# Optimization experiments

Hardware: AMD Instinct MI355X
Metric: run time of the kernel (lower is better)

The kernel has to match this reference:

```python
import jax, jax.numpy as jnp
import numpy as np

B, T, C = 2, 2048, 4096
NH, NKV, HD = 32, 8, 128
GROUPS = NH // NKV
THETA = 10000.0


def _rope_tables(seq_len, dim, theta, dtype):
    inv_freq = 1.0 / (theta ** (jnp.arange(0, dim, 2, dtype=jnp.float32) / dim))
    t = jnp.arange(seq_len, dtype=jnp.float32)
    freqs = jnp.outer(t, inv_freq)            # [T, dim/2]
    emb = jnp.concatenate([freqs, freqs], -1)  # [T, dim]
    return jnp.cos(emb).astype(dtype), jnp.sin(emb).astype(dtype)


def _rotate_half(x):
    h = x.shape[-1] // 2
    return jnp.concatenate([-x[..., h:], x[..., :h]], axis=-1)


def setup_inputs() -> dict:
    key = jax.random.key(0)
    ks = jax.random.split(key, 5)
    s = 1.0 / np.sqrt(C)
    return {
        "x": jax.random.normal(ks[0], (B, T, C), jnp.float32),
        "wq": jax.random.normal(ks[1], (C, NH * HD), jnp.float32) * s,
        "wk": jax.random.normal(ks[2], (C, NKV * HD), jnp.float32) * s,
        "wv": jax.random.normal(ks[3], (C, NKV * HD), jnp.float32) * s,
        "wo": jax.random.normal(ks[4], (NH * HD, C), jnp.float32) * s,
    }


def reference(x, wq, wk, wv, wo):
    b, t, c = x.shape
    q = (x @ wq).reshape(b, t, NH, HD).transpose(0, 2, 1, 3)    # [B,NH,T,HD]
    k = (x @ wk).reshape(b, t, NKV, HD).transpose(0, 2, 1, 3)   # [B,NKV,T,HD]
    v = (x @ wv).reshape(b, t, NKV, HD).transpose(0, 2, 1, 3)
    cos, sin = _rope_tables(t, HD, THETA, x.dtype)              # [T,HD]
    cos = cos[None, None]
    sin = sin[None, None]
    q = q * cos + _rotate_half(q) * sin
    k = k * cos + _rotate_half(k) * sin
    # GQA: broadcast KV heads over groups via einsum instead of materializing repeat
    qg = q.reshape(b, NKV, GROUPS, t, HD)
    scores = jnp.einsum('bkgqd,bkld->bkgql', qg, k) * (HD ** -0.5)  # [B,NKV,G,T,T]
    causal = jnp.triu(jnp.full((t, t), -jnp.inf, dtype=x.dtype), k=1)
    scores = scores + causal
    attn = jax.nn.softmax(scores, axis=-1)
    out = jnp.einsum('bkgql,bkld->bkgqd', attn, v)              # [B,NKV,G,T,HD]
    out = out.reshape(b, NH, t, HD).transpose(0, 2, 1, 3).reshape(b, t, NH * HD)
    return out @ wo
```

## Files before the change

kernel.cpp:

```cpp
#include <hip/hip_runtime.h>
#include <hip/hip_bf16.h>
#include <math.h>

#define B_ 2
#define T_ 2048
#define C_ 4096
#define NH_ 32
#define NKV_ 8
#define HD_ 128
#define M_ (B_*T_)
#define QKVN_ (NH_*HD_ + 2*NKV_*HD_)

using bf16 = __hip_bfloat16;
typedef __bf16 bf16x8 __attribute__((ext_vector_type(8)));
typedef float f32x4 __attribute__((ext_vector_type(4)));

__device__ inline f32x4 mfma16(bf16x8 a, bf16x8 b, f32x4 c) {
    return __builtin_amdgcn_mfma_f32_16x16x32_bf16(a, b, c, 0, 0, 0);
}

__global__ __launch_bounds__(256) void cast_f32_bf16(const float* __restrict__ in,
                                                     bf16* __restrict__ out, int n4) {
    int i = blockIdx.x * 256 + threadIdx.x;
    if (i >= n4) return;
    float4 v = reinterpret_cast<const float4*>(in)[i];
    union { bf16 h[4]; uint2 u; } o;
    o.h[0] = __float2bfloat16(v.x);
    o.h[1] = __float2bfloat16(v.y);
    o.h[2] = __float2bfloat16(v.z);
    o.h[3] = __float2bfloat16(v.w);
    reinterpret_cast<uint2*>(out)[i] = o.u;
}

__global__ __launch_bounds__(256) void transpose_cast(const float* __restrict__ in,
                                                      bf16* __restrict__ out, int K, int N) {
    __shared__ float tile[32][33];
    int tx = threadIdx.x & 31, ty = threadIdx.x >> 5;
    int n0 = blockIdx.x << 5, k0 = blockIdx.y << 5;
#pragma unroll
    for (int p = 0; p < 4; ++p)
        tile[p*8 + ty][tx] = in[(size_t)(k0 + p*8 + ty) * N + n0 + tx];
    __syncthreads();
#pragma unroll
    for (int p = 0; p < 4; ++p)
        out[(size_t)(n0 + p*8 + ty) * K + k0 + tx] = __float2bfloat16(tile[tx][p*8 + ty]);
}

__device__ inline void store_out(float* p, float v) { *p = v; }
__device__ inline void store_out(bf16*  p, float v) { *p = __float2bfloat16(v); }

template <typename OutT>
__global__ __launch_bounds__(512, 2) void gemm256(const bf16* __restrict__ A,
                                                  const bf16* __restrict__ Bt,
                                                  OutT* __restrict__ C,
                                                  int M, int N, int K) {
    __shared__ __align__(16) char lds[131072];
    const int tid = threadIdx.x;
    const int wid = tid >> 6, lane = tid & 63;
    const int lq = lane & 15, lg = lane >> 4;
    const int wrow = wid >> 2, wcol = wid & 3;

    const int nwg = gridDim.x;
    const int q8 = nwg >> 3;
    const int wg = (blockIdx.x & 7) * q8 + (blockIdx.x >> 3);
    const int nby = M >> 8;
    const int by = wg % nby, bx = wg / nby;
    const int brow = by << 8, bcol = bx << 8;

    const bf16* Ag = A + (size_t)brow * K;
    const bf16* Bg = Bt + (size_t)bcol * K;
    const int nt = K >> 6;

    const int srow = (wid << 3) + (lane >> 3);
    const int schunk = (lane & 7) ^ ((lane >> 3) & 7);

#define STAGE_HALF(gbase, ldsoff, t2, cbuf, hf)                                         \
    {                                                                                   \
        _Pragma("unroll")                                                               \
        for (int l = 0; l < 2; ++l) {                                                   \
            const int r0 = (hf) * 128 + l * 64;                                         \
            const char* src = (const char*)(gbase) +                                    \
                ((size_t)(r0 + srow) * K + (size_t)(t2) * 64) * 2 + schunk * 16;        \
            char* dst = &lds[(ldsoff) + (cbuf) * 32768 + (r0 + (wid << 3)) * 128];      \
            __builtin_amdgcn_global_load_lds(                                           \
                (const __attribute__((address_space(1))) void*)src,                     \
                (__attribute__((address_space(3))) void*)dst, 16, 0, 0);                \
        }                                                                               \
    }

#define LDA(cbuf, mh, mf, ks) \
    (*(const bf16x8*)&lds[(cbuf)*32768 + (wrow*128 + (mh)*64 + (mf)*16 + lq)*128 + ((((ks)*4 + lg)) ^ (lq & 7))*16])
#define LDB(cbuf, nh, nf, ks) \
    (*(const bf16x8*)&lds[65536 + (cbuf)*32768 + (wcol*64 + (nh)*32 + (nf)*16 + lq)*128 + ((((ks)*4 + lg)) ^ (lq & 7))*16])

#define READ_A(cbuf, mh) \
    { _Pragma("unroll") for (int mf = 0; mf < 4; ++mf) { a[mf][0] = LDA(cbuf, mh, mf, 0); a[mf][1] = LDA(cbuf, mh, mf, 1); } }
#define READ_B(cbuf, nh, breg) \
    { _Pragma("unroll") for (int nf = 0; nf < 2; ++nf) { breg[nf][0] = LDB(cbuf, nh, nf, 0); breg[nf][1] = LDB(cbuf, nh, nf, 1); } }
#define MFMA_Q(am, an, breg)                                                     \
    { __builtin_amdgcn_s_setprio(1);                                             \
      _Pragma("unroll") for (int mf = 0; mf < 4; ++mf)                           \
          _Pragma("unroll") for (int nf = 0; nf < 2; ++nf)                       \
              _Pragma("unroll") for (int ks = 0; ks < 2; ++ks)                   \
                  acc[(am) + mf][(an) + nf] = mfma16(a[mf][ks], breg[nf][ks],    \
                                                     acc[(am) + mf][(an) + nf]); \
      __builtin_amdgcn_s_setprio(0); }
#define BAR() __builtin_amdgcn_s_barrier()

    f32x4 acc[8][4] = {};
    bf16x8 a[4][2], b0[2][2], b1[2][2];

    STAGE_HALF(Ag, 0,     0, 0, 0); STAGE_HALF(Ag, 0,     0, 0, 1);
    STAGE_HALF(Bg, 65536, 0, 0, 0); STAGE_HALF(Bg, 65536, 0, 0, 1);
    STAGE_HALF(Bg, 65536, 1, 1, 0); STAGE_HALF(Bg, 65536, 1, 1, 1);
    asm volatile("s_waitcnt vmcnt(4)" ::: "memory");
    BAR();

    for (int i = 0; i < (nt >> 1); ++i) {
        const int u = 2 * i;
        const bool s_u2 = (u + 2) < nt;
        const bool s_v2 = (u + 3) < nt;

        READ_A(0, 0); READ_B(0, 0, b0);
        STAGE_HALF(Ag, 0, u + 1, 1, 0);
        MFMA_Q(0, 0, b0);
        BAR();
        READ_B(0, 1, b1);
        STAGE_HALF(Ag, 0, u + 1, 1, 1);
        MFMA_Q(0, 2, b1);
        BAR();
        READ_A(0, 1);
        if (s_u2) STAGE_HALF(Bg, 65536, u + 2, 0, 0);
        MFMA_Q(4, 2, b1);
        BAR();
        if (s_u2) STAGE_HALF(Bg, 65536, u + 2, 0, 1);
        MFMA_Q(4, 0, b0);
        if (s_u2) asm volatile("s_waitcnt vmcnt(4)" ::: "memory");
        else      asm volatile("s_waitcnt vmcnt(0)" ::: "memory");
        BAR();
        READ_A(1, 0); READ_B(1, 0, b0);
        if (s_u2) STAGE_HALF(Ag, 0, u + 2, 0, 0);
        MFMA_Q(0, 0, b0);
        BAR();
        READ_B(1, 1, b1);
        if (s_u2) STAGE_HALF(Ag, 0, u + 2, 0, 1);
        MFMA_Q(0, 2, b1);
        BAR();
        READ_A(1, 1);
        if (s_v2) STAGE_HALF(Bg, 65536, u + 3, 1, 0);
        MFMA_Q(4, 2, b1);
        BAR();
        if (s_v2) STAGE_HALF(Bg, 65536, u + 3, 1, 1);
        MFMA_Q(4, 0, b0);
        if (s_v2) asm volatile("s_waitcnt vmcnt(4)" ::: "memory");
        else      asm volatile("s_waitcnt vmcnt(0)" ::: "memory");
        BAR();
    }
#undef STAGE_HALF
#undef LDA
#undef LDB
#undef READ_A
#undef READ_B
#undef MFMA_Q
#undef BAR

#pragma unroll
    for (int mf = 0; mf < 8; ++mf)
#pragma unroll
        for (int nf = 0; nf < 4; ++nf)
#pragma unroll
            for (int r = 0; r < 4; ++r) {
                int row = brow + wrow * 128 + mf * 16 + lg * 4 + r;
                int col = bcol + wcol * 64 + nf * 16 + lq;
                store_out(&C[(size_t)row * N + col], acc[mf][nf][r]);
            }
}

__global__ __launch_bounds__(256) void rope_qk(const bf16* __restrict__ qkv,
                                               bf16* __restrict__ outp,
                                               int nheads, int col_off, float qscale) {
    size_t idx = (size_t)blockIdx.x * 256 + threadIdx.x;
    int i = (int)(idx & 63);
    size_t rest = idx >> 6;
    int t = (int)(rest % T_);
    rest /= T_;
    int hh = (int)(rest % nheads);
    int b = (int)(rest / nheads);

    const bf16* src = qkv + (size_t)(b * T_ + t) * QKVN_ + col_off + hh * HD_;
    float x0 = __bfloat162float(src[i]);
    float x1 = __bfloat162float(src[i + 64]);
    float inv = exp2f((float)i * -0.20762050593045952f);
    float th = (float)t * inv;
    float s = sinf(th), c = cosf(th);
    bf16* dst = outp + ((size_t)(b * nheads + hh) * T_ + t) * HD_;
    dst[i]      = __float2bfloat16((x0 * c - x1 * s) * qscale);
    dst[i + 64] = __float2bfloat16((x1 * c + x0 * s) * qscale);
}

__global__ __launch_bounds__(256) void vtrans(const bf16* __restrict__ qkv,
                                              bf16* __restrict__ vt) {
    __shared__ bf16 tile[32][33];
    int gx = blockIdx.x;
    int dt = gx & 3;
    int tt = (gx >> 2) & 63;
    int kv = (gx >> 8) & 7;
    int b  = gx >> 11;
    int d0 = dt * 32, t0 = tt * 32;
    int tx = threadIdx.x & 31, ty = threadIdx.x >> 5;

    const bf16* src = qkv + (size_t)(b * T_ + t0) * QKVN_ + (NH_*HD_ + NKV_*HD_) + kv * HD_ + d0;
#pragma unroll
    for (int p = 0; p < 4; ++p)
        tile[p*8 + ty][tx] = src[(size_t)(p*8 + ty) * QKVN_ + tx];
    __syncthreads();
    bf16* dst = vt + ((size_t)((b * NKV_ + kv) * HD_ + d0)) * T_ + t0;
#pragma unroll
    for (int p = 0; p < 4; ++p)
        dst[(size_t)(p*8 + ty) * T_ + tx] = tile[tx][p*8 + ty];
}

__global__ __launch_bounds__(1024) void fattn(const bf16* __restrict__ Q,
                                              const bf16* __restrict__ Kt,
                                              const bf16* __restrict__ VT,
                                              bf16* __restrict__ O) {
    const int lin = blockIdx.x;
    const int kv = lin & 7;
    const int b  = (lin >> 3) & 1;
    const int idx = lin >> 4;
    const int h  = kv * 4 + (idx & 3);
    const int jp = idx >> 2;

    const int tid = threadIdx.x, wid = tid >> 6, lane = tid & 63;
    const int lq = lane & 15, lg = lane >> 4;

    const bf16* Kp = Kt + (size_t)(b * NKV_ + kv) * T_ * HD_;
    const bf16* Vp = VT + (size_t)(b * NKV_ + kv) * HD_ * T_;

    __shared__ __align__(16) bf16 Ks[2][64][128];
    __shared__ __align__(16) bf16 Vs[2][128][64];
    __shared__ __align__(16) bf16 p_lds[16][16][72];

    const float THR_L2 = 11.5416f;

#define STAGE_KV(cbuf, tt)                                                           \
    { {                                                                              \
        int krow = wid * 4 + (lane >> 4);                                            \
        int kch  = (lane & 15) ^ (krow & 15);                                        \
        const bf16* ksrc = Kp + (size_t)((tt) * 64 + krow) * HD_ + kch * 8;          \
        __builtin_amdgcn_global_load_lds(                                            \
            (const __attribute__((address_space(1))) void*)ksrc,                     \
            (__attribute__((address_space(3))) void*)&Ks[cbuf][wid*4][0],            \
            16, 0, 0);                                                               \
      }                                                                              \
      {                                                                              \
        int vrow = wid * 8 + (lane >> 3);                                            \
        int vch  = (lane & 7) ^ (vrow & 7);                                          \
        const bf16* vsrc = Vp + (size_t)vrow * T_ + (tt) * 64 + vch * 8;             \
        __builtin_amdgcn_global_load_lds(                                            \
            (const __attribute__((address_space(1))) void*)vsrc,                     \
            (__attribute__((address_space(3))) void*)&Vs[cbuf][wid*8][0],            \
            16, 0, 0);                                                               \
      } }

    for (int half = 0; half < 2; ++half) {
        const int qt = half ? (7 - jp) : jp;
        const int q0 = qt * 256 + wid * 16;
        const int kv_end = q0 + 16;
        const int NT = qt * 4 + 4;

        const bf16* Qp = Q + ((size_t)(b * NH_ + h) * T_ + q0) * HD_;
        bf16x8 qf[4];
#pragma unroll
        for (int c = 0; c < 4; ++c)
            qf[c] = *(const bf16x8*)&Qp[(size_t)lq * HD_ + c * 32 + lg * 8];

        f32x4 oacc[8] = {};
        float m_r = -INFINITY;
        float l_r = 0.f;

        STAGE_KV(0, 0);
        STAGE_KV(1, 1);
        asm volatile("s_waitcnt vmcnt(2)" ::: "memory");
        __builtin_amdgcn_s_barrier();

        for (int t = 0; t < NT; ++t) {
            const int cb = t & 1;
            const int t0 = t * 64;

            if (t0 < kv_end) {
                f32x4 st[4] = {};
#pragma unroll
                for (int n = 0; n < 4; ++n) {
                    bf16x8 kf[4];
#pragma unroll
                    for (int c = 0; c < 4; ++c)
                        kf[c] = *(const bf16x8*)((const char*)&Ks[cb][n*16 + lq][0]
                                                  + (((c*4 + lg) ^ lq) << 4));
                    __builtin_amdgcn_s_setprio(1);
#pragma unroll
                    for (int c = 0; c < 4; ++c)
                        st[n] = mfma16(kf[c], qf[c], st[n]);
                    __builtin_amdgcn_s_setprio(0);
                }

                const int qq = q0 + lq;
#pragma unroll
                for (int n = 0; n < 4; ++n)
#pragma unroll
                    for (int r = 0; r < 4; ++r) {
                        int kk = t0 + n*16 + lg*4 + r;
                        if (kk > qq) st[n][r] = -INFINITY;
                    }

                float rmax = st[0][0];
#pragma unroll
                for (int n = 0; n < 4; ++n)
#pragma unroll
                    for (int r = 0; r < 4; ++r) rmax = fmaxf(rmax, st[n][r]);
                rmax = fmaxf(rmax, __shfl_xor(rmax, 16));
                rmax = fmaxf(rmax, __shfl_xor(rmax, 32));

                if (__any(rmax - m_r > THR_L2)) {
                    float mnew = fmaxf(m_r, rmax);
                    float alpha = exp2f(m_r - mnew);
                    m_r = mnew;
                    l_r *= alpha;
#pragma unroll
                    for (int r = 0; r < 4; ++r) {
                        float a_pv = __shfl(alpha, lg*4 + r);
#pragma unroll
                        for (int f = 0; f < 8; ++f) oacc[f][r] *= a_pv;
                    }
                }

                float rsum = 0.f;
#pragma unroll
                for (int n = 0; n < 4; ++n)
#pragma unroll
                    for (int r = 0; r < 4; ++r) {
                        float p = exp2f(st[n][r] - m_r);
                        st[n][r] = p;
                        rsum += p;
                    }
                rsum += __shfl_xor(rsum, 16);
                rsum += __shfl_xor(rsum, 32);
                l_r += rsum;

#pragma unroll
                for (int n = 0; n < 4; ++n) {
                    union { bf16 hh[4]; uint2 u; } pk;
#pragma unroll
                    for (int r = 0; r < 4; ++r) pk.hh[r] = __float2bfloat16(st[n][r]);
                    *(uint2*)&p_lds[wid][lq][n*16 + lg*4] = pk.u;
                }

#pragma unroll
                for (int ks = 0; ks < 2; ++ks) {
                    bf16x8 pa = *(const bf16x8*)&p_lds[wid][lq][ks*32 + lg*8];
                    bf16x8 vf[8];
#pragma unroll
                    for (int f = 0; f < 8; ++f)
                        vf[f] = *(const bf16x8*)((const char*)&Vs[cb][f*16 + lq][0]
                                                  + (((ks*4 + lg) ^ (lq & 7)) << 4));
                    __builtin_amdgcn_s_setprio(1);
#pragma unroll
                    for (int f = 0; f < 8; ++f)
                        oacc[f] = mfma16(pa, vf[f], oacc[f]);
                    __builtin_amdgcn_s_setprio(0);
                }
            }

            __builtin_amdgcn_s_barrier();
            if (t + 2 < NT) {
                STAGE_KV(cb, t + 2);
                asm volatile("s_waitcnt vmcnt(2)" ::: "memory");
            } else {
                asm volatile("s_waitcnt vmcnt(0)" ::: "memory");
            }
            __builtin_amdgcn_s_barrier();
        }

        {
            float rinv = __builtin_amdgcn_rcpf(l_r);
#pragma unroll
            for (int r = 0; r < 4; ++r) {
                float rl = __shfl(rinv, lg*4 + r);
                int row = q0 + lg*4 + r;
#pragma unroll
                for (int f = 0; f < 8; ++f) {
                    int d = f*16 + lq;
                    O[((size_t)(b * T_ + row) * NH_ + h) * HD_ + d] =
                        __float2bfloat16(oacc[f][r] * rl);
                }
            }
        }
    }
#undef STAGE_KV
}

extern "C" void kernel_launch(void* const* d_in, const int* in_sizes, int n_in,
                              void* d_out, int out_size, void* d_ws, size_t ws_size,
                              hipStream_t stream) {
    const float* x  = (const float*)d_in[0];
    const float* wq = (const float*)d_in[1];
    const float* wk = (const float*)d_in[2];
    const float* wv = (const float*)d_in[3];
    const float* wo = (const float*)d_in[4];
    float* out = (float*)d_out;

    bf16* ws    = (bf16*)d_ws;
    bf16* xb    = ws;
    bf16* wqkvT = xb + (size_t)M_ * C_;
    bf16* woT   = wqkvT + (size_t)QKVN_ * C_;
    bf16* qkv   = woT + (size_t)C_ * C_;

    bf16* attn = xb;
    bf16* q_r  = wqkvT;
    bf16* k_r  = q_r + (size_t)B_ * NH_ * T_ * HD_;
    bf16* vt   = k_r + (size_t)B_ * NKV_ * T_ * HD_;

    cast_f32_bf16<<<(M_ * C_ / 4 + 255) / 256, 256, 0, stream>>>(x, xb, M_ * C_ / 4);
    transpose_cast<<<dim3(128, 128), 256, 0, stream>>>(wq, wqkvT, C_, NH_ * HD_);
    transpose_cast<<<dim3(32, 128), 256, 0, stream>>>(wk, wqkvT + (size_t)(NH_ * HD_) * C_, C_, NKV_ * HD_);
    transpose_cast<<<dim3(32, 128), 256, 0, stream>>>(wv, wqkvT + (size_t)(NH_ * HD_ + NKV_ * HD_) * C_, C_, NKV_ * HD_);
    transpose_cast<<<dim3(128, 128), 256, 0, stream>>>(wo, woT, NH_ * HD_, C_);

    gemm256<bf16><<<dim3((QKVN_ / 256) * (M_ / 256)), 512, 0, stream>>>(xb, wqkvT, qkv, M_, QKVN_, C_);

    rope_qk<<<(B_ * NH_ * T_ * 64) / 256, 256, 0, stream>>>(qkv, q_r, NH_, 0, 0.12751741230963214f);
    rope_qk<<<(B_ * NKV_ * T_ * 64) / 256, 256, 0, stream>>>(qkv, k_r, NKV_, NH_ * HD_, 1.0f);
    vtrans<<<B_ * NKV_ * (T_ / 32) * (HD_ / 32), 256, 0, stream>>>(qkv, vt);

    fattn<<<dim3(256), 1024, 0, stream>>>(q_r, k_r, vt, attn);

    gemm256<float><<<dim3((C_ / 256) * (M_ / 256)), 512, 0, stream>>>(attn, woT, out, M_, C_, C_);
}
```

Baseline: 521.7 us.

## Fuse RoPE into QKV GEMM epilogue and deepen GEMM prefetch waits

Adds a gemm_qkv kernel that remaps the B-tile columns so each wave holds both halves of a rotary pair. RoPE and the query scale are applied in the epilogue, which writes Q and K straight to head-major layout, and V goes to a compact buffer. This removes the separate rope_qk passes and the full bf16 QKV round trip, and a small precomputed cos/sin table replaces per-element trig. The shared GEMM loop now waits on vmcnt(8) instead of vmcnt(4), allowing more loads in flight. The wo transpose moves after attention so its buffer can be reused for Q, and the scattered epilogue stores may be less coalesced.

After: 502.0 us. 3.8% less time.

```diff
diff --git a/kernel.cpp b/kernel.cpp
--- a/kernel.cpp
+++ b/kernel.cpp
@@ -46,32 +46,79 @@
         out[(size_t)(n0 + p*8 + ty) * K + k0 + tx] = __float2bfloat16(tile[tx][p*8 + ty]);
 }
 
-__device__ inline void store_out(float* p, float v) { *p = v; }
-__device__ inline void store_out(bf16*  p, float v) { *p = __float2bfloat16(v); }
-
-template <typename OutT>
-__global__ __launch_bounds__(512, 2) void gemm256(const bf16* __restrict__ A,
-                                                  const bf16* __restrict__ Bt,
-                                                  OutT* __restrict__ C,
-                                                  int M, int N, int K) {
-    __shared__ __align__(16) char lds[131072];
-    const int tid = threadIdx.x;
-    const int wid = tid >> 6, lane = tid & 63;
-    const int lq = lane & 15, lg = lane >> 4;
-    const int wrow = wid >> 2, wcol = wid & 3;
-
-    const int nwg = gridDim.x;
-    const int q8 = nwg >> 3;
-    const int wg = (blockIdx.x & 7) * q8 + (blockIdx.x >> 3);
-    const int nby = M >> 8;
-    const int by = wg % nby, bx = wg / nby;
-    const int brow = by << 8, bcol = bx << 8;
-
-    const bf16* Ag = A + (size_t)brow * K;
-    const bf16* Bg = Bt + (size_t)bcol * K;
-    const int nt = K >> 6;
-
-    const int srow = (wid << 3) + (lane >> 3);
+__global__ __launch_bounds__(256) void rope_tab(float2* __restrict__ tab) {
+    int idx = blockIdx.x * 256 + threadIdx.x;
+    int i = idx & 63, t = idx >> 6;
+    float inv = exp2f((float)i * -0.20762050593045952f);
+    float th = (float)t * inv;
+    tab[idx] = make_float2(cosf(th), sinf(th));
+}
+
+#define GEMM_PROLOG_AND_LOOP(LDB_ROW_EXPR)                                              \
+    f32x4 acc[8][4] = {};                                                               \
+    bf16x8 a[4][2], b0[2][2], b1[2][2];                                                 \
+    STAGE_HALF(Ag, 0,     0, 0, 0); STAGE_HALF(Ag, 0,     0, 0, 1);                     \
+    STAGE_HALF(Bg, 65536, 0, 0, 0); STAGE_HALF(Bg, 65536, 0, 0, 1);                     \
+    STAGE_HALF(Bg, 65536, 1, 1, 0); STAGE_HALF(Bg, 65536, 1, 1, 1);                     \
+    asm volatile("s_waitcnt vmcnt(4)" ::: "memory");                                    \
+    BAR();                                                                              \
+    for (int it = 0; it < (nt >> 1); ++it) {                                            \
+        const int u = 2 * it;                                                           \
+        const bool more = (u + 2) < nt;                                                 \
+        READ_A(0, 0); READ_B(0, 0, b0);                                                 \
+        STAGE_HALF(Ag, 0, u + 1, 1, 0);                                                 \
+        MFMA_Q(0, 0, b0);                                                               \
+        BAR();                                                                          \
+        READ_B(0, 1, b1);                                                               \
+        STAGE_HALF(Ag, 0, u + 1, 1, 1);                                                 \
+        MFMA_Q(0, 2, b1);                                                               \
+        BAR();                                                                          \
+        READ_A(0, 1);                                                                   \
+        if (more) STAGE_HALF(Bg, 65536, u + 2, 0, 0);                                   \
+        MFMA_Q(4, 2, b1);                                                               \
+        BAR();                                                                          \
+        if (more) STAGE_HALF(Bg, 65536, u + 2, 0, 1);                                   \
+        MFMA_Q(4, 0, b0);                                                               \
+        if (more) asm volatile("s_waitcnt vmcnt(8)" ::: "memory");                      \
+        else      asm volatile("s_waitcnt vmcnt(4)" ::: "memory");                      \
+        BAR();                                                                          \
+        READ_A(1, 0); READ_B(1, 0, b0);                                                 \
+        if (more) STAGE_HALF(Ag, 0, u + 2, 0, 0);                                       \
+        MFMA_Q(0, 0, b0);                                                               \
+        BAR();                                                                          \
+        READ_B(1, 1, b1);                                                               \
+        if (more) STAGE_HALF(Ag, 0, u + 2, 0, 1);                                       \
+        MFMA_Q(0, 2, b1);                                                               \
+        if (more) asm volatile("s_waitcnt vmcnt(8)" ::: "memory");                      \
+        else      asm volatile("s_waitcnt vmcnt(0)" ::: "memory");                      \
+        BAR();                                                                          \
+        READ_A(1, 1);                                                                   \
+        if (more) STAGE_HALF(Bg, 65536, u + 3, 1, 0);                                   \
+        MFMA_Q(4, 2, b1);                                                               \
+        BAR();                                                                          \
+        if (more) STAGE_HALF(Bg, 65536, u + 3, 1, 1);                                   \
+        MFMA_Q(4, 0, b0);                                                               \
+        if (more) asm volatile("s_waitcnt vmcnt(4)" ::: "memory");                      \
+        else      asm volatile("s_waitcnt vmcnt(0)" ::: "memory");                      \
+        BAR();                                                                          \
+    }
+
+#define GEMM_COMMON_DEFS                                                                \
+    __shared__ __align__(16) char lds[131072];                                          \
+    const int tid = threadIdx.x;                                                        \
+    const int wid = tid >> 6, lane = tid & 63;                                          \
+    const int lq = lane & 15, lg = lane >> 4;                                           \
+    const int wrow = wid >> 2, wcol = wid & 3;                                          \
+    const int nwg = gridDim.x;                                                          \
+    const int q8 = nwg >> 3;                                                            \
+    const int wg = (blockIdx.x & 7) * q8 + (blockIdx.x >> 3);                           \
+    const int nby = M >> 8;                                                             \
+    const int by = wg % nby, bx = wg / nby;                                             \
+    const int brow = by << 8, bcol = bx << 8;                                           \
+    const bf16* Ag = A + (size_t)brow * K;                                              \
+    const bf16* Bg = Bt + (size_t)bcol * K;                                             \
+    const int nt = K >> 6;                                                              \
+    const int srow = (wid << 3) + (lane >> 3);                                          \
     const int schunk = (lane & 7) ^ ((lane >> 3) & 7);
 
 #define STAGE_HALF(gbase, ldsoff, t2, cbuf, hf)                                         \
@@ -90,8 +137,6 @@
 
 #define LDA(cbuf, mh, mf, ks) \
     (*(const bf16x8*)&lds[(cbuf)*32768 + (wrow*128 + (mh)*64 + (mf)*16 + lq)*128 + ((((ks)*4 + lg)) ^ (lq & 7))*16])
-#define LDB(cbuf, nh, nf, ks) \
-    (*(const bf16x8*)&lds[65536 + (cbuf)*32768 + (wcol*64 + (nh)*32 + (nf)*16 + lq)*128 + ((((ks)*4 + lg)) ^ (lq & 7))*16])
 
 #define READ_A(cbuf, mh) \
     { _Pragma("unroll") for (int mf = 0; mf < 4; ++mf) { a[mf][0] = LDA(cbuf, mh, mf, 0); a[mf][1] = LDA(cbuf, mh, mf, 1); } }
@@ -107,63 +152,19 @@
       __builtin_amdgcn_s_setprio(0); }
 #define BAR() __builtin_amdgcn_s_barrier()
 
-    f32x4 acc[8][4] = {};
-    bf16x8 a[4][2], b0[2][2], b1[2][2];
-
-    STAGE_HALF(Ag, 0,     0, 0, 0); STAGE_HALF(Ag, 0,     0, 0, 1);
-    STAGE_HALF(Bg, 65536, 0, 0, 0); STAGE_HALF(Bg, 65536, 0, 0, 1);
-    STAGE_HALF(Bg, 65536, 1, 1, 0); STAGE_HALF(Bg, 65536, 1, 1, 1);
-    asm volatile("s_waitcnt vmcnt(4)" ::: "memory");
-    BAR();
-
-    for (int i = 0; i < (nt >> 1); ++i) {
-        const int u = 2 * i;
-        const bool s_u2 = (u + 2) < nt;
-        const bool s_v2 = (u + 3) < nt;
-
-        READ_A(0, 0); READ_B(0, 0, b0);
-        STAGE_HALF(Ag, 0, u + 1, 1, 0);
-        MFMA_Q(0, 0, b0);
-        BAR();
-        READ_B(0, 1, b1);
-        STAGE_HALF(Ag, 0, u + 1, 1, 1);
-        MFMA_Q(0, 2, b1);
-        BAR();
-        READ_A(0, 1);
-        if (s_u2) STAGE_HALF(Bg, 65536, u + 2, 0, 0);
-        MFMA_Q(4, 2, b1);
-        BAR();
-        if (s_u2) STAGE_HALF(Bg, 65536, u + 2, 0, 1);
-        MFMA_Q(4, 0, b0);
-        if (s_u2) asm volatile("s_waitcnt vmcnt(4)" ::: "memory");
-        else      asm volatile("s_waitcnt vmcnt(0)" ::: "memory");
-        BAR();
-        READ_A(1, 0); READ_B(1, 0, b0);
-        if (s_u2) STAGE_HALF(Ag, 0, u + 2, 0, 0);
-        MFMA_Q(0, 0, b0);
-        BAR();
-        READ_B(1, 1, b1);
-        if (s_u2) STAGE_HALF(Ag, 0, u + 2, 0, 1);
-        MFMA_Q(0, 2, b1);
-        BAR();
-        READ_A(1, 1);
-        if (s_v2) STAGE_HALF(Bg, 65536, u + 3, 1, 0);
-        MFMA_Q(4, 2, b1);
-        BAR();
-        if (s_v2) STAGE_HALF(Bg, 65536, u + 3, 1, 1);
-        MFMA_Q(4, 0, b0);
-        if (s_v2) asm volatile("s_waitcnt vmcnt(4)" ::: "memory");
-        else      asm volatile("s_waitcnt vmcnt(0)" ::: "memory");
-        BAR();
-    }
-#undef STAGE_HALF
-#undef LDA
+__device__ inline void store_out(float* p, float v) { *p = v; }
+__device__ inline void store_out(bf16*  p, float v) { *p = __float2bfloat16(v); }
+
+template <typename OutT>
+__global__ __launch_bounds__(512, 2) void gemm256(const bf16* __restrict__ A,
+                                                  const bf16* __restrict__ Bt,
+                                                  OutT* __restrict__ C,
+                                                  int M, int N, int K) {
+    GEMM_COMMON_DEFS
+#define LDB(cbuf, nh, nf, ks) \
+    (*(const bf16x8*)&lds[65536 + (cbuf)*32768 + (wcol*64 + (nh)*32 + (nf)*16 + lq)*128 + ((((ks)*4 + lg)) ^ (lq & 7))*16])
+    GEMM_PROLOG_AND_LOOP(plain)
 #undef LDB
-#undef READ_A
-#undef READ_B
-#undef MFMA_Q
-#undef BAR
-
 #pragma unroll
     for (int mf = 0; mf < 8; ++mf)
 #pragma unroll
@@ -176,29 +177,74 @@
             }
 }
 
-__global__ __launch_bounds__(256) void rope_qk(const bf16* __restrict__ qkv,
-                                               bf16* __restrict__ outp,
-                                               int nheads, int col_off, float qscale) {
-    size_t idx = (size_t)blockIdx.x * 256 + threadIdx.x;
-    int i = (int)(idx & 63);
-    size_t rest = idx >> 6;
-    int t = (int)(rest % T_);
-    rest /= T_;
-    int hh = (int)(rest % nheads);
-    int b = (int)(rest / nheads);
-
-    const bf16* src = qkv + (size_t)(b * T_ + t) * QKVN_ + col_off + hh * HD_;
-    float x0 = __bfloat162float(src[i]);
-    float x1 = __bfloat162float(src[i + 64]);
-    float inv = exp2f((float)i * -0.20762050593045952f);
-    float th = (float)t * inv;
-    float s = sinf(th), c = cosf(th);
-    bf16* dst = outp + ((size_t)(b * nheads + hh) * T_ + t) * HD_;
-    dst[i]      = __float2bfloat16((x0 * c - x1 * s) * qscale);
-    dst[i + 64] = __float2bfloat16((x1 * c + x0 * s) * qscale);
-}
-
-__global__ __launch_bounds__(256) void vtrans(const bf16* __restrict__ qkv,
+__global__ __launch_bounds__(512, 2) void gemm_qkv(const bf16* __restrict__ A,
+                                                   const bf16* __restrict__ Bt,
+                                                   bf16* __restrict__ q_r,
+                                                   bf16* __restrict__ k_r,
+                                                   bf16* __restrict__ vbuf,
+                                                   const float2* __restrict__ tab,
+                                                   int M, int N, int K) {
+    GEMM_COMMON_DEFS
+#define LDB(cbuf, nh, nf, ks) \
+    (*(const bf16x8*)&lds[65536 + (cbuf)*32768 + (((wcol>>1)*128 + (wcol&1)*32 + (nh)*64 + (nf)*16 + lq))*128 + ((((ks)*4 + lg)) ^ (lq & 7))*16])
+    GEMM_PROLOG_AND_LOOP(remap)
+#undef LDB
+
+    const int trow = brow + wrow * 128;
+    if (bcol >= 5120) {
+#pragma unroll
+        for (int mf = 0; mf < 8; ++mf)
+#pragma unroll
+            for (int j = 0; j < 4; ++j)
+#pragma unroll
+                for (int r = 0; r < 4; ++r) {
+                    int row = trow + mf*16 + lg*4 + r;
+                    int col = bcol + (wcol>>1)*128 + (wcol&1)*32 + (j>>1)*64 + (j&1)*16 + lq;
+                    vbuf[(size_t)row * (NKV_*HD_) + (col - 5120)] = __float2bfloat16(acc[mf][j][r]);
+                }
+    } else {
+        const bool isQ = (bcol < 4096);
+        const float sc = isQ ? 0.12751741230963214f : 1.0f;
+#pragma unroll
+        for (int mf = 0; mf < 8; ++mf)
+#pragma unroll
+            for (int j = 0; j < 2; ++j)
+#pragma unroll
+                for (int r = 0; r < 4; ++r) {
+                    int row = trow + mf*16 + lg*4 + r;
+                    int bb = row >> 11, tt = row & 2047;
+                    int i  = (wcol&1)*32 + j*16 + lq;
+                    float2 cs = tab[tt*64 + i];
+                    float x0 = acc[mf][j][r], x1 = acc[mf][j+2][r];
+                    float y0 = (x0*cs.x - x1*cs.y) * sc;
+                    float y1 = (x1*cs.x + x0*cs.y) * sc;
+                    int col0 = bcol + (wcol>>1)*128 + i;
+                    if (isQ) {
+                        int h = col0 >> 7, hd = col0 & 127;
+                        bf16* dst = q_r + ((size_t)(bb*NH_ + h)*T_ + tt)*HD_;
+                        dst[hd]      = __float2bfloat16(y0);
+                        dst[hd + 64] = __float2bfloat16(y1);
+                    } else {
+                        int ch = col0 - 4096;
+                        int h = ch >> 7, hd = ch & 127;
+                        bf16* dst = k_r + ((size_t)(bb*NKV_ + h)*T_ + tt)*HD_;
+                        dst[hd]      = __float2bfloat16(y0);
+                        dst[hd + 64] = __float2bfloat16(y1);
+                    }
+                }
+    }
+}
+
+#undef GEMM_PROLOG_AND_LOOP
+#undef GEMM_COMMON_DEFS
+#undef STAGE_HALF
+#undef LDA
+#undef READ_A
+#undef READ_B
+#undef MFMA_Q
+#undef BAR
+
+__global__ __launch_bounds__(256) void vtrans(const bf16* __restrict__ vbuf,
                                               bf16* __restrict__ vt) {
     __shared__ bf16 tile[32][33];
     int gx = blockIdx.x;
@@ -209,10 +255,10 @@
     int d0 = dt * 32, t0 = tt * 32;
     int tx = threadIdx.x & 31, ty = threadIdx.x >> 5;
 
-    const bf16* src = qkv + (size_t)(b * T_ + t0) * QKVN_ + (NH_*HD_ + NKV_*HD_) + kv * HD_ + d0;
+    const bf16* src = vbuf + (size_t)(b * T_ + t0) * (NKV_*HD_) + kv * HD_ + d0;
 #pragma unroll
     for (int p = 0; p < 4; ++p)
-        tile[p*8 + ty][tx] = src[(size_t)(p*8 + ty) * QKVN_ + tx];
+        tile[p*8 + ty][tx] = src[(size_t)(p*8 + ty) * (NKV_*HD_) + tx];
     __syncthreads();
     bf16* dst = vt + ((size_t)((b * NKV_ + kv) * HD_ + d0)) * T_ + t0;
 #pragma unroll
@@ -412,27 +458,28 @@
     bf16* ws    = (bf16*)d_ws;
     bf16* xb    = ws;
     bf16* wqkvT = xb + (size_t)M_ * C_;
-    bf16* woT   = wqkvT + (size_t)QKVN_ * C_;
-    bf16* qkv   = woT + (size_t)C_ * C_;
+    bf16* qr_wo = wqkvT + (size_t)QKVN_ * C_;
+    bf16* region = qr_wo + (size_t)C_ * C_;
+    bf16* k_r  = region;
+    bf16* vt   = k_r + (size_t)B_ * NKV_ * T_ * HD_;
+    bf16* vbuf = vt  + (size_t)B_ * NKV_ * T_ * HD_;
+    float2* tab = (float2*)(vbuf + (size_t)B_ * T_ * NKV_ * HD_);
 
     bf16* attn = xb;
-    bf16* q_r  = wqkvT;
-    bf16* k_r  = q_r + (size_t)B_ * NH_ * T_ * HD_;
-    bf16* vt   = k_r + (size_t)B_ * NKV_ * T_ * HD_;
 
     cast_f32_bf16<<<(M_ * C_ / 4 + 255) / 256, 256, 0, stream>>>(x, xb, M_ * C_ / 4);
     transpose_cast<<<dim3(128, 128), 256, 0, stream>>>(wq, wqkvT, C_, NH_ * HD_);
     transpose_cast<<<dim3(32, 128), 256, 0, stream>>>(wk, wqkvT + (size_t)(NH_ * HD_) * C_, C_, NKV_ * HD_);
     transpose_cast<<<dim3(32, 128), 256, 0, stream>>>(wv, wqkvT + (size_t)(NH_ * HD_ + NKV_ * HD_) * C_, C_, NKV_ * HD_);
-    transpose_cast<<<dim3(128, 128), 256, 0, stream>>>(wo, woT, NH_ * HD_, C_);
-
-    gemm256<bf16><<<dim3((QKVN_ / 256) * (M_ / 256)), 512, 0, stream>>>(xb, wqkvT, qkv, M_, QKVN_, C_);
-
-    rope_qk<<<(B_ * NH_ * T_ * 64) / 256, 256, 0, stream>>>(qkv, q_r, NH_, 0, 0.12751741230963214f);
-    rope_qk<<<(B_ * NKV_ * T_ * 64) / 256, 256, 0, stream>>>(qkv, k_r, NKV_, NH_ * HD_, 1.0f);
-    vtrans<<<B_ * NKV_ * (T_ / 32) * (HD_ / 32), 256, 0, stream>>>(qkv, vt);
-
-    fattn<<<dim3(256), 1024, 0, stream>>>(q_r, k_r, vt, attn);
-
-    gemm256<float><<<dim3((C_ / 256) * (M_ / 256)), 512, 0, stream>>>(attn, woT, out, M_, C_, C_);
-}
+    rope_tab<<<(T_ * 64) / 256, 256, 0, stream>>>(tab);
+
+    gemm_qkv<<<dim3((QKVN_ / 256) * (M_ / 256)), 512, 0, stream>>>(
+        xb, wqkvT, qr_wo, k_r, vbuf, tab, M_, QKVN_, C_);
+
+    vtrans<<<B_ * NKV_ * (T_ / 32) * (HD_ / 32), 256, 0, stream>>>(vbuf, vt);
+
+    fattn<<<dim3(256), 1024, 0, stream>>>(qr_wo, k_r, vt, attn);
+
+    transpose_cast<<<dim3(128, 128), 256, 0, stream>>>(wo, qr_wo, NH_ * HD_, C_);
+    gemm256<float><<<dim3((C_ / 256) * (M_ / 256)), 512, 0, stream>>>(attn, qr_wo, out, M_, C_, C_);
+}
```
